# Kernel optimization log

Measured on AMD Instinct MI355X. Metric: run time of the kernel, lower is better.

The kernel has to match this reference:

```python
import jax, jax.numpy as jnp
import numpy as np

NCODEBOOKS, K, SUBVEC = 32, 16, 128
IN_F, OUT_F = 4096, 2048
BATCH, SEQ = 2, 1024


def setup_inputs() -> dict:
    key = jax.random.key(0)
    k1, k2, k3, k4, k5 = jax.random.split(key, 5)
    return {
        "x": jax.random.normal(k1, (BATCH, SEQ, IN_F), dtype=jnp.float32),
        "centroids": jax.random.normal(k2, (NCODEBOOKS, K, SUBVEC), dtype=jnp.float32),
        "weight": jax.random.normal(k3, (NCODEBOOKS, SUBVEC, OUT_F), dtype=jnp.float32),
        "inverse_temperature_logit": jax.random.normal(k4, (1,), dtype=jnp.float32),
        "bias": jax.random.normal(k5, (OUT_F,), dtype=jnp.float32),
    }


def reference(x, centroids, weight, inverse_temperature_logit, bias):
    shape = x.shape[:-1]
    C, k, d = centroids.shape
    # [N, C, d] -> [C, N, d]
    xr = jnp.transpose(x.reshape(-1, C, d), (1, 0, 2))
    # Euclidean cdist per codebook: [C, N, k]
    x2 = jnp.sum(xr * xr, axis=-1)[:, :, None]
    c2 = jnp.sum(centroids * centroids, axis=-1)[:, None, :]
    xc = jnp.einsum('cnd,ckd->cnk', xr, centroids)
    dist = jnp.sqrt(jnp.maximum(x2 + c2 - 2.0 * xc, 0.0))
    inv_temp = jax.nn.softplus(inverse_temperature_logit) + 1.0  # [1]
    attention = jax.nn.softmax(-dist * inv_temp, axis=-1)  # [C, N, k]
    lut = jnp.einsum('ckd,cdo->cko', centroids, weight)  # [C, k, O]
    training_output = jnp.einsum('cnk,cko->no', attention, lut)  # [N, O]
    # one-hot argmin matmul == direct gather of lut rows
    idx = jnp.argmin(dist, axis=-1)  # [C, N]
    gathered = jnp.take_along_axis(lut, idx[:, :, None], axis=1)  # [C, N, O]
    inference_output = jnp.sum(gathered, axis=0)  # [N, O]
    # straight-through estimator
    output = training_output - jax.lax.stop_gradient(training_output - inference_output)
    output = output + bias
    return output.reshape(*shape, lut.shape[-1])
```

## Files before the change

### kernel.cpp

```cpp
#include <hip/hip_runtime.h>

#define NCB 32
#define KK 16
#define DD 128
#define IN_F 4096
#define OUT_F 2048
#define NTOK 2048

__global__ __launch_bounds__(256) void lut_kernel(const float* __restrict__ centroids,
                                                  const float* __restrict__ weight,
                                                  float* __restrict__ lut,
                                                  float* __restrict__ c2out) {
    const int c = blockIdx.y;
    const int o0 = blockIdx.x * 64;
    const int lane_o = threadIdx.x & 63;
    const int dg = threadIdx.x >> 6;
    __shared__ float cent[KK * DD];
    __shared__ float part[4][KK][64];

    const float4* cbase = (const float4*)(centroids + (size_t)c * KK * DD);
    float4* cs4 = (float4*)cent;
    for (int i = threadIdx.x; i < KK * DD / 4; i += 256) cs4[i] = cbase[i];
    __syncthreads();

    if (blockIdx.x == 0 && threadIdx.x < KK) {
        float s = 0.f;
        for (int d = 0; d < DD; ++d) { float v = cent[threadIdx.x * DD + d]; s += v * v; }
        c2out[c * KK + threadIdx.x] = s;
    }

    float acc[KK];
#pragma unroll
    for (int k = 0; k < KK; ++k) acc[k] = 0.f;
    const float* wbase = weight + (size_t)c * DD * OUT_F + o0 + lane_o;
#pragma unroll
    for (int chunk = 0; chunk < 8; ++chunk) {
        const int d = dg * 32 + chunk * 4;
        float w0 = wbase[(size_t)(d + 0) * OUT_F];
        float w1 = wbase[(size_t)(d + 1) * OUT_F];
        float w2 = wbase[(size_t)(d + 2) * OUT_F];
        float w3 = wbase[(size_t)(d + 3) * OUT_F];
#pragma unroll
        for (int k = 0; k < KK; ++k) {
            float4 cv = *(const float4*)(cent + k * DD + d);
            acc[k] += cv.x * w0 + cv.y * w1 + cv.z * w2 + cv.w * w3;
        }
    }
#pragma unroll
    for (int k = 0; k < KK; ++k) part[dg][k][lane_o] = acc[k];
    __syncthreads();
#pragma unroll
    for (int r = 0; r < 4; ++r) {
        int i = r * 256 + threadIdx.x;
        int k = i >> 6, o = i & 63;
        float s = part[0][k][o] + part[1][k][o] + part[2][k][o] + part[3][k][o];
        lut[((size_t)c * KK + k) * OUT_F + o0 + o] = s;
    }
}

__global__ __launch_bounds__(256) void idx_kernel(const float* __restrict__ x,
                                                  const float* __restrict__ centroids,
                                                  const float* __restrict__ c2,
                                                  unsigned char* __restrict__ idxout) {
    const int t = blockIdx.x;
    const int k = threadIdx.x >> 4;
    const int j = threadIdx.x & 15;
    __shared__ float xs[IN_F];
    __shared__ float dproxy[NCB * KK];

    {
        const float4* xg = (const float4*)(x + (size_t)t * IN_F);
        float4* xs4 = (float4*)xs;
        for (int i = threadIdx.x; i < IN_F / 4; i += 256) xs4[i] = xg[i];
    }
    __syncthreads();

    for (int c = 0; c < NCB; ++c) {
        const float4* cg = (const float4*)(centroids + ((size_t)c * KK + k) * DD + j * 8);
        float4 c0 = cg[0], c1 = cg[1];
        const float4* xv = (const float4*)(xs + c * DD + j * 8);
        float4 x0 = xv[0], x1 = xv[1];
        float dot = c0.x * x0.x + c0.y * x0.y + c0.z * x0.z + c0.w * x0.w
                  + c1.x * x1.x + c1.y * x1.y + c1.z * x1.z + c1.w * x1.w;
#pragma unroll
        for (int s = 1; s < 16; s <<= 1) dot += __shfl_xor(dot, s);
        if (j == 0) dproxy[c * KK + k] = c2[c * KK + k] - 2.f * dot;
    }
    __syncthreads();

    if (threadIdx.x < NCB) {
        const float* dp = dproxy + threadIdx.x * KK;
        float best = dp[0];
        int bi = 0;
#pragma unroll
        for (int kk = 1; kk < KK; ++kk) {
            float v = dp[kk];
            if (v < best) { best = v; bi = kk; }
        }
        idxout[(size_t)t * NCB + threadIdx.x] = (unsigned char)bi;
    }
}

__global__ __launch_bounds__(256) void gather_kernel(const float* __restrict__ lut,
                                                     const unsigned char* __restrict__ idxb,
                                                     const float* __restrict__ bias,
                                                     float* __restrict__ out) {
    const int t0 = blockIdx.x * 128;
    const int o0 = blockIdx.y * 32;
    __shared__ float slut[NCB * KK * 32];
    __shared__ unsigned char sidx[128 * NCB];

    {
        const int row = threadIdx.x >> 3;
        const int q = threadIdx.x & 7;
        for (int r = row; r < NCB * KK; r += 32)
            ((float4*)(slut + r * 32))[q] = ((const float4*)(lut + (size_t)r * OUT_F + o0))[q];
    }
    {
        const int4* ig = (const int4*)(idxb + (size_t)t0 * NCB);
        int4* is4 = (int4*)sidx;
        if (threadIdx.x < 256) is4[threadIdx.x] = ig[threadIdx.x];
    }
    __syncthreads();

    const int oo = (threadIdx.x & 15) * 2;
    const int tl = threadIdx.x >> 4;
    const float2 bv = *(const float2*)(bias + o0 + oo);

    for (int tt = tl; tt < 128; tt += 16) {
        float2 acc = bv;
        const unsigned int* ip = (const unsigned int*)(sidx + tt * NCB);
#pragma unroll
        for (int c4 = 0; c4 < NCB / 4; ++c4) {
            unsigned int iv4 = ip[c4];
#pragma unroll
            for (int b = 0; b < 4; ++b) {
                int c = c4 * 4 + b;
                int iv = (iv4 >> (8 * b)) & 0xff;
                const float2 v = *(const float2*)(slut + (c * KK + iv) * 32 + oo);
                acc.x += v.x;
                acc.y += v.y;
            }
        }
        *(float2*)(out + (size_t)(t0 + tt) * OUT_F + o0 + oo) = acc;
    }
}

extern "C" void kernel_launch(void* const* d_in, const int* in_sizes, int n_in,
                              void* d_out, int out_size, void* d_ws, size_t ws_size,
                              hipStream_t stream) {
    const float* x         = (const float*)d_in[0];
    const float* centroids = (const float*)d_in[1];
    const float* weight    = (const float*)d_in[2];
    const float* bias      = (const float*)d_in[4];
    float* out = (float*)d_out;

    float* lut = (float*)d_ws;
    unsigned char* idxb = (unsigned char*)d_ws + (4u << 20);
    float* c2 = (float*)((char*)d_ws + (4u << 20) + (64u << 10));

    lut_kernel<<<dim3(OUT_F / 64, NCB), 256, 0, stream>>>(centroids, weight, lut, c2);
    idx_kernel<<<NTOK, 256, 0, stream>>>(x, centroids, c2, idxb);
    gather_kernel<<<dim3(NTOK / 128, OUT_F / 32), 256, 0, stream>>>(lut, idxb, bias, out);
}
```

Baseline: 155.2 us.

## Retile idx kernel per codebook, read centroids from global in LUT, pad gather LUT

The idx kernel now runs one block per (64-token tile, codebook). It stages that codebook's centroids in padded shared memory and computes a 4x4 register tile of token-by-centroid dots, then takes the argmin across threads with shuffles. This replaces the per-token block that staged the whole x row. The LUT kernel drops its shared-memory centroid copy and reads centroids straight from global/cache. The gather kernel processes 256 tokens per block with a padded (36-stride) shared LUT to cut bank conflicts, which adds LDS use and may reduce occupancy.

```diff
diff --git a/kernel.cpp b/kernel.cpp
--- a/kernel.cpp
+++ b/kernel.cpp
@@ -15,17 +15,12 @@
     const int o0 = blockIdx.x * 64;
     const int lane_o = threadIdx.x & 63;
     const int dg = threadIdx.x >> 6;
-    __shared__ float cent[KK * DD];
     __shared__ float part[4][KK][64];
 
-    const float4* cbase = (const float4*)(centroids + (size_t)c * KK * DD);
-    float4* cs4 = (float4*)cent;
-    for (int i = threadIdx.x; i < KK * DD / 4; i += 256) cs4[i] = cbase[i];
-    __syncthreads();
-
     if (blockIdx.x == 0 && threadIdx.x < KK) {
+        const float* cb = centroids + ((size_t)c * KK + threadIdx.x) * DD;
         float s = 0.f;
-        for (int d = 0; d < DD; ++d) { float v = cent[threadIdx.x * DD + d]; s += v * v; }
+        for (int d = 0; d < DD; ++d) { float v = cb[d]; s += v * v; }
         c2out[c * KK + threadIdx.x] = s;
     }
 
@@ -33,6 +28,7 @@
 #pragma unroll
     for (int k = 0; k < KK; ++k) acc[k] = 0.f;
     const float* wbase = weight + (size_t)c * DD * OUT_F + o0 + lane_o;
+    const float* cbase = centroids + (size_t)c * KK * DD;
 #pragma unroll
     for (int chunk = 0; chunk < 8; ++chunk) {
         const int d = dg * 32 + chunk * 4;
@@ -42,7 +38,7 @@
         float w3 = wbase[(size_t)(d + 3) * OUT_F];
 #pragma unroll
         for (int k = 0; k < KK; ++k) {
-            float4 cv = *(const float4*)(cent + k * DD + d);
+            float4 cv = *(const float4*)(cbase + k * DD + d);
             acc[k] += cv.x * w0 + cv.y * w1 + cv.z * w2 + cv.w * w3;
         }
     }
@@ -61,43 +57,80 @@
 __global__ __launch_bounds__(256) void idx_kernel(const float* __restrict__ x,
                                                   const float* __restrict__ centroids,
                                                   const float* __restrict__ c2,
-                                                  unsigned char* __restrict__ idxout) {
-    const int t = blockIdx.x;
-    const int k = threadIdx.x >> 4;
-    const int j = threadIdx.x & 15;
-    __shared__ float xs[IN_F];
-    __shared__ float dproxy[NCB * KK];
+                                                  unsigned char* __restrict__ idxb) {
+    const int c = blockIdx.y;
+    const int t0 = blockIdx.x * 64;
+    const int tid = threadIdx.x;
+    const int th_q = tid & 3;
+    const int th_k = (tid >> 2) & 3;
+    const int th_t = tid >> 4;
 
-    {
-        const float4* xg = (const float4*)(x + (size_t)t * IN_F);
-        float4* xs4 = (float4*)xs;
-        for (int i = threadIdx.x; i < IN_F / 4; i += 256) xs4[i] = xg[i];
+    __shared__ float cent_s[KK * 164];
+
+    for (int p = tid; p < KK * 32; p += 256) {
+        int k = p >> 5, f4 = p & 31;
+        int q = f4 >> 3, jj = f4 & 7;
+        *(float4*)(cent_s + k * 164 + q * 40 + jj * 4) =
+            *(const float4*)(centroids + ((size_t)c * KK + k) * DD + f4 * 4);
     }
     __syncthreads();
 
-    for (int c = 0; c < NCB; ++c) {
-        const float4* cg = (const float4*)(centroids + ((size_t)c * KK + k) * DD + j * 8);
-        float4 c0 = cg[0], c1 = cg[1];
-        const float4* xv = (const float4*)(xs + c * DD + j * 8);
-        float4 x0 = xv[0], x1 = xv[1];
-        float dot = c0.x * x0.x + c0.y * x0.y + c0.z * x0.z + c0.w * x0.w
-                  + c1.x * x1.x + c1.y * x1.y + c1.z * x1.z + c1.w * x1.w;
+    float c2v[4];
 #pragma unroll
-        for (int s = 1; s < 16; s <<= 1) dot += __shfl_xor(dot, s);
-        if (j == 0) dproxy[c * KK + k] = c2[c * KK + k] - 2.f * dot;
+    for (int kk = 0; kk < 4; ++kk) c2v[kk] = c2[c * KK + th_k * 4 + kk];
+
+    float acc[4][4];
+#pragma unroll
+    for (int r = 0; r < 4; ++r)
+#pragma unroll
+        for (int kk = 0; kk < 4; ++kk) acc[r][kk] = 0.f;
+
+    const float* xb0 = x + (size_t)(t0 + th_t * 4) * IN_F + c * DD + th_q * 32;
+#pragma unroll
+    for (int chunk = 0; chunk < 8; ++chunk) {
+        float4 xa[4];
+#pragma unroll
+        for (int r = 0; r < 4; ++r)
+            xa[r] = *(const float4*)(xb0 + (size_t)r * IN_F + chunk * 4);
+        float4 ca[4];
+#pragma unroll
+        for (int kk = 0; kk < 4; ++kk)
+            ca[kk] = *(const float4*)(cent_s + (th_k * 4 + kk) * 164 + th_q * 40 + chunk * 4);
+#pragma unroll
+        for (int r = 0; r < 4; ++r)
+#pragma unroll
+            for (int kk = 0; kk < 4; ++kk)
+                acc[r][kk] += xa[r].x * ca[kk].x + xa[r].y * ca[kk].y
+                            + xa[r].z * ca[kk].z + xa[r].w * ca[kk].w;
     }
-    __syncthreads();
 
-    if (threadIdx.x < NCB) {
-        const float* dp = dproxy + threadIdx.x * KK;
-        float best = dp[0];
-        int bi = 0;
 #pragma unroll
-        for (int kk = 1; kk < KK; ++kk) {
-            float v = dp[kk];
-            if (v < best) { best = v; bi = kk; }
+    for (int r = 0; r < 4; ++r)
+#pragma unroll
+        for (int kk = 0; kk < 4; ++kk) {
+            float a = acc[r][kk];
+            a += __shfl_xor(a, 1);
+            a += __shfl_xor(a, 2);
+            acc[r][kk] = a;
         }
-        idxout[(size_t)t * NCB + threadIdx.x] = (unsigned char)bi;
+
+#pragma unroll
+    for (int r = 0; r < 4; ++r) {
+        float best = c2v[0] - 2.f * acc[r][0];
+        int bi = th_k * 4;
+#pragma unroll
+        for (int kk = 1; kk < 4; ++kk) {
+            float v = c2v[kk] - 2.f * acc[r][kk];
+            if (v < best) { best = v; bi = th_k * 4 + kk; }
+        }
+#pragma unroll
+        for (int s = 4; s <= 8; s <<= 1) {
+            float ov = __shfl_xor(best, s);
+            int oi = __shfl_xor(bi, s);
+            if (ov < best || (ov == best && oi < bi)) { best = ov; bi = oi; }
+        }
+        if ((tid & 15) == 0)
+            idxb[(size_t)(t0 + th_t * 4 + r) * NCB + c] = (unsigned char)bi;
     }
 }
 
@@ -105,21 +138,22 @@
                                                      const unsigned char* __restrict__ idxb,
                                                      const float* __restrict__ bias,
                                                      float* __restrict__ out) {
-    const int t0 = blockIdx.x * 128;
+    const int t0 = blockIdx.x * 256;
     const int o0 = blockIdx.y * 32;
-    __shared__ float slut[NCB * KK * 32];
-    __shared__ unsigned char sidx[128 * NCB];
+    __shared__ float slut[NCB * KK * 36];
+    __shared__ unsigned char sidx[256 * NCB];
 
     {
         const int row = threadIdx.x >> 3;
         const int q = threadIdx.x & 7;
         for (int r = row; r < NCB * KK; r += 32)
-            ((float4*)(slut + r * 32))[q] = ((const float4*)(lut + (size_t)r * OUT_F + o0))[q];
+            *(float4*)(slut + r * 36 + q * 4) =
+                *(const float4*)(lut + (size_t)r * OUT_F + o0 + q * 4);
     }
     {
         const int4* ig = (const int4*)(idxb + (size_t)t0 * NCB);
         int4* is4 = (int4*)sidx;
-        if (threadIdx.x < 256) is4[threadIdx.x] = ig[threadIdx.x];
+        for (int i = threadIdx.x; i < 512; i += 256) is4[i] = ig[i];
     }
     __syncthreads();
 
@@ -127,7 +161,7 @@
     const int tl = threadIdx.x >> 4;
     const float2 bv = *(const float2*)(bias + o0 + oo);
 
-    for (int tt = tl; tt < 128; tt += 16) {
+    for (int tt = tl; tt < 256; tt += 16) {
         float2 acc = bv;
         const unsigned int* ip = (const unsigned int*)(sidx + tt * NCB);
 #pragma unroll
@@ -135,9 +169,9 @@
             unsigned int iv4 = ip[c4];
 #pragma unroll
             for (int b = 0; b < 4; ++b) {
-                int c = c4 * 4 + b;
+                int cc = c4 * 4 + b;
                 int iv = (iv4 >> (8 * b)) & 0xff;
-                const float2 v = *(const float2*)(slut + (c * KK + iv) * 32 + oo);
+                const float2 v = *(const float2*)(slut + (cc * KK + iv) * 36 + oo);
                 acc.x += v.x;
                 acc.y += v.y;
             }
@@ -160,6 +194,6 @@
     float* c2 = (float*)((char*)d_ws + (4u << 20) + (64u << 10));
 
     lut_kernel<<<dim3(OUT_F / 64, NCB), 256, 0, stream>>>(centroids, weight, lut, c2);
-    idx_kernel<<<NTOK, 256, 0, stream>>>(x, centroids, c2, idxb);
-    gather_kernel<<<dim3(NTOK / 128, OUT_F / 32), 256, 0, stream>>>(lut, idxb, bias, out);
+    idx_kernel<<<dim3(NTOK / 64, NCB), 256, 0, stream>>>(x, centroids, c2, idxb);
+    gather_kernel<<<dim3(NTOK / 256, OUT_F / 32), 256, 0, stream>>>(lut, idxb, bias, out);
 }
```

Measured after the change: 163.1 us. +5.0%, slower.
